# Optimization experiments

Hardware: AMD Instinct MI355X
Metric: run time of the kernel (lower is better)

Reference implementation:

```python
import jax, jax.numpy as jnp
import numpy as np

N, H, C = 16384, 32, 128
RADIUS = 1.0
SIGMA = 1.0
SHELL_SIZES = [1, 14, 28]
EPS = 1e-5


def make_kernel_points(radius, shell_sizes, dim=3, seed=42):
    """Deterministic kernel point dispositions: one center point, then shells of
    unit-direction points at increasing radii (fixed buffer, like load_kernels)."""
    rng = np.random.RandomState(seed)
    shell_radii = np.linspace(0.0, radius, len(shell_sizes))
    pts = [np.zeros((shell_sizes[0], dim))]
    for s, r in zip(shell_sizes[1:], shell_radii[1:]):
        d = rng.randn(s, dim)
        d /= np.linalg.norm(d, axis=1, keepdims=True)
        pts.append(d * r)
    return np.concatenate(pts, 0).astype(np.float32)  # (K, dim)


_KP = jnp.asarray(make_kernel_points(RADIUS, SHELL_SIZES))  # (43, 3)


def batch_norm(x, gamma, beta):
    # BatchNorm1d in training mode over the point/batch axis, biased variance.
    mean = jnp.mean(x, axis=0)
    var = jnp.mean(jnp.square(x - mean), axis=0)
    return (x - mean) * jax.lax.rsqrt(var + EPS) * gamma + beta


def setup_inputs() -> dict:
    key = jax.random.key(0)
    ks = jax.random.split(key, 8)
    coord = jax.random.normal(ks[0], (N, 3), dtype=jnp.float32)
    feat = jax.random.normal(ks[1], (N, C), dtype=jnp.float32)
    offset = jnp.array([N], dtype=jnp.int64)
    reference_index = jax.random.randint(ks[2], (N, H), 0, N, dtype=jnp.int64)
    fc1_w = jax.random.normal(ks[3], (C, C), dtype=jnp.float32) * 0.02
    fc3_w = jax.random.normal(ks[4], (C, C), dtype=jnp.float32) * 0.02
    conv_w = jax.random.normal(ks[5], (43, C), dtype=jnp.float32) * 0.1
    ones = jnp.ones((C,), dtype=jnp.float32)
    zeros = jnp.zeros((C,), dtype=jnp.float32)
    return {
        "coord": coord, "feat": feat, "offset": offset,
        "reference_index": reference_index,
        "fc1_w": fc1_w, "fc3_w": fc3_w, "conv_w": conv_w,
        "g1": ones, "b1": zeros, "g2": ones, "b2": zeros, "g3": ones, "b3": zeros,
    }


def reference(coord, feat, offset, reference_index, fc1_w, fc3_w, conv_w,
              g1, b1, g2, b2, g3, b3):
    identity = feat
    # fc1 -> BN -> ReLU
    x = jax.nn.relu(batch_norm(feat @ fc1_w.T, g1, b1))

    # ---- KPConvD (depthwise kernel point conv, Cmid=0) ----
    # shadow point far away / shadow feature = 0 for out-of-range neighbor index N
    s_pts = jnp.concatenate([coord, jnp.full((1, 3), 1e6, coord.dtype)], axis=0)
    s_feats = jnp.concatenate([x, jnp.zeros((1, C), x.dtype)], axis=0)
    neighbors = s_pts[reference_index] - coord[:, None, :]          # (N, H, 3)
    diff = neighbors[:, :, None, :] - _KP[None, None, :, :]          # (N, H, K, 3)
    sq_d = jnp.sum(diff * diff, axis=-1)                             # (N, H, K)
    infl = jnp.clip(1.0 - jnp.sqrt(sq_d) / SIGMA, 0.0, None)         # (N, H, K) linear influence
    nfeats = s_feats[reference_index]                                # (N, H, C) neighbor gather
    weighted = jnp.einsum('nhk,nhc->nkc', infl, nfeats)              # (N, K, C)
    x = jnp.sum(weighted * conv_w[None], axis=1)                     # depthwise sum over K -> (N, C)

    # BN -> ReLU
    x = jax.nn.relu(batch_norm(x, g2, b2))
    # fc3 -> BN
    x = batch_norm(x @ fc3_w.T, g3, b3)
    # residual + ReLU (drop_path_rate=0 -> identity)
    feat_out = jax.nn.relu(identity + x)
    return coord, feat_out, offset
```

## Files before the change

kernel.cpp:

```cpp
#include <hip/hip_runtime.h>
#include <math.h>

#define NPTS 16384
#define NH   32
#define NC   128
#define NK   43

typedef __attribute__((ext_vector_type(8))) short short8;
typedef __attribute__((ext_vector_type(4))) float f32x4;

enum : int {
  OFF_W1PK = 0,
  OFF_W3PK = 8192,
  OFF_CWPK = 16384,
  OFF_KPF  = 20480,
  OFF_SC1  = 20736, OFF_SH1 = 20864,
  OFF_SC2  = 20992, OFF_SH2 = 21120,
  OFF_SC3  = 21248, OFF_SH3 = 21376,
  OFF_RED  = 21504,
  OFF_CNT  = 29696,
  OFF_PART = 29952,
  OFF_A    = 1078528,
  OFF_B    = 1078528 + NPTS*NC,
};

struct KPArgs { float p[NK * 3]; };

static void host_make_kp(float* kp) {
  unsigned int mt[624];
  mt[0] = 42u;
  for (int i = 1; i < 624; ++i)
    mt[i] = 1812433253u * (mt[i-1] ^ (mt[i-1] >> 30)) + (unsigned)i;
  int pos = 624;
  auto next = [&]() -> unsigned int {
    if (pos == 624) {
      for (int i = 0; i < 624; ++i) {
        unsigned int y = (mt[i] & 0x80000000u) | (mt[(i+1)%624] & 0x7fffffffu);
        unsigned int v = mt[(i+397)%624] ^ (y >> 1);
        if (y & 1u) v ^= 0x9908b0dfu;
        mt[i] = v;
      }
      pos = 0;
    }
    unsigned int y = mt[pos++];
    y ^= y >> 11;
    y ^= (y << 7)  & 0x9d2c5680u;
    y ^= (y << 15) & 0xefc60000u;
    y ^= y >> 18;
    return y;
  };
  auto rdouble = [&]() -> double {
    unsigned int a = next() >> 5, b = next() >> 6;
    return ((double)a * 67108864.0 + (double)b) / 9007199254740992.0;
  };
  double gcache = 0.0; bool has_g = false;
  auto gauss = [&]() -> double {
    if (has_g) { has_g = false; return gcache; }
    double x1, x2, r2;
    do {
      x1 = 2.0 * rdouble() - 1.0;
      x2 = 2.0 * rdouble() - 1.0;
      r2 = x1*x1 + x2*x2;
    } while (r2 >= 1.0 || r2 == 0.0);
    double f = sqrt(-2.0 * log(r2) / r2);
    gcache = f * x1; has_g = true;
    return f * x2;
  };
  double g[126];
  for (int i = 0; i < 126; ++i) g[i] = gauss();
  kp[0] = 0.f; kp[1] = 0.f; kp[2] = 0.f;
  for (int r = 0; r < 14; ++r) {
    double x = g[r*3], y = g[r*3+1], z = g[r*3+2];
    double nrm = sqrt(x*x + y*y + z*z);
    kp[(1+r)*3+0] = (float)(x / nrm * 0.5);
    kp[(1+r)*3+1] = (float)(y / nrm * 0.5);
    kp[(1+r)*3+2] = (float)(z / nrm * 0.5);
  }
  for (int r = 0; r < 28; ++r) {
    double x = g[42+r*3], y = g[42+r*3+1], z = g[42+r*3+2];
    double nrm = sqrt(x*x + y*y + z*z);
    kp[(15+r)*3+0] = (float)(x / nrm);
    kp[(15+r)*3+1] = (float)(y / nrm);
    kp[(15+r)*3+2] = (float)(z / nrm);
  }
}

__device__ __forceinline__ unsigned short f2bf(float f) {
  unsigned u = __float_as_uint(f);
  return (unsigned short)((u + 0x7FFFu + ((u >> 16) & 1u)) >> 16);
}
__device__ __forceinline__ unsigned pack_bf_trunc(float a, float b) {
  return __builtin_amdgcn_perm(__float_as_uint(b), __float_as_uint(a), 0x07060302);
}

__global__ __launch_bounds__(256) void prep_kernel(
    const float* __restrict__ w1, const float* __restrict__ w3,
    const float* __restrict__ cw, KPArgs kpa,
    uint4* __restrict__ w1pk, uint4* __restrict__ w3pk,
    uint4* __restrict__ cwpk, float* __restrict__ kpf,
    unsigned* __restrict__ cnt) {
  int idx = blockIdx.x * 256 + threadIdx.x;
  if (idx == 0) *cnt = 0u;
  if (idx < 4096) {
    int mat = idx >> 11, t = idx & 2047;
    int f = t >> 6, l = t & 63;
    int nt = f >> 2, ks = f & 3;
    int c = nt*16 + (l & 15), k0 = ks*32 + (l >> 4)*8;
    const float* src = mat ? w3 : w1;
    const float* p = src + (size_t)c * NC + k0;
    uint4 q;
    q.x = (unsigned)f2bf(p[0]) | ((unsigned)f2bf(p[1]) << 16);
    q.y = (unsigned)f2bf(p[2]) | ((unsigned)f2bf(p[3]) << 16);
    q.z = (unsigned)f2bf(p[4]) | ((unsigned)f2bf(p[5]) << 16);
    q.w = (unsigned)f2bf(p[6]) | ((unsigned)f2bf(p[7]) << 16);
    (mat ? w3pk : w1pk)[f*64 + l] = q;
  } else if (idx < 4096 + 1024) {
    int t = idx - 4096;
    int f = t >> 6, l = t & 63;
    int ks = f >> 3, nt = f & 7;
    int c = nt*16 + (l & 15), k0 = ks*32 + (l >> 4)*8;
    float v[8];
    #pragma unroll
    for (int i = 0; i < 8; ++i) {
      int k = k0 + i;
      v[i] = (k < NK) ? cw[k*NC + c] : 0.f;
    }
    uint4 q;
    q.x = (unsigned)f2bf(v[0]) | ((unsigned)f2bf(v[1]) << 16);
    q.y = (unsigned)f2bf(v[2]) | ((unsigned)f2bf(v[3]) << 16);
    q.z = (unsigned)f2bf(v[4]) | ((unsigned)f2bf(v[5]) << 16);
    q.w = (unsigned)f2bf(v[6]) | ((unsigned)f2bf(v[7]) << 16);
    cwpk[f*64 + l] = q;
  } else if (idx < 4096 + 1024 + 256) {
    int t = idx - (4096 + 1024);
    int comp = t >> 6, slot = t & 63;
    int ks = slot >> 5, g = (slot >> 3) & 3, i = slot & 7;
    int k = ks*32 + g*8 + i;
    float val;
    if (k < NK) {
      float x = kpa.p[k*3+0], y = kpa.p[k*3+1], z = kpa.p[k*3+2];
      val = (comp == 0) ? -2.f*x : (comp == 1) ? -2.f*y : (comp == 2) ? -2.f*z
            : (x*x + y*y + z*z);
    } else {
      val = (comp == 3) ? 1e12f : 0.f;
    }
    kpf[comp*64 + slot] = val;
  }
}

template<int BN>
__global__ __launch_bounds__(64) void gemm_mfma(
    const float* __restrict__ A, const uint4* __restrict__ Wpk,
    const float* __restrict__ sc, const float* __restrict__ sh,
    float* __restrict__ out, float* __restrict__ part) {
  int l = threadIdx.x;
  int li = l & 15, g = l >> 4;
  const float* arow = A + (size_t)(blockIdx.x * 16 + li) * NC;

  short8 afr[4];
  #pragma unroll
  for (int ks = 0; ks < 4; ++ks) {
    int k0 = ks*32 + g*8;
    float4 a0 = *(const float4*)(arow + k0);
    float4 a1 = *(const float4*)(arow + k0 + 4);
    float v[8] = {a0.x,a0.y,a0.z,a0.w,a1.x,a1.y,a1.z,a1.w};
    if (BN) {
      float4 s0 = *(const float4*)(sc + k0), s1 = *(const float4*)(sc + k0 + 4);
      float4 h0 = *(const float4*)(sh + k0), h1 = *(const float4*)(sh + k0 + 4);
      float ss[8] = {s0.x,s0.y,s0.z,s0.w,s1.x,s1.y,s1.z,s1.w};
      float hh[8] = {h0.x,h0.y,h0.z,h0.w,h1.x,h1.y,h1.z,h1.w};
      #pragma unroll
      for (int i = 0; i < 8; ++i) v[i] = fmaxf(0.f, fmaf(v[i], ss[i], hh[i]));
    }
    union { unsigned q[4]; short8 s; } pk;
    #pragma unroll
    for (int p = 0; p < 4; ++p) pk.q[p] = pack_bf_trunc(v[2*p], v[2*p+1]);
    afr[ks] = pk.s;
  }

  f32x4 acc[8];
  #pragma unroll
  for (int nt = 0; nt < 8; ++nt) acc[nt] = (f32x4){0.f,0.f,0.f,0.f};
  #pragma unroll
  for (int nt = 0; nt < 8; ++nt) {
    #pragma unroll
    for (int ks = 0; ks < 4; ++ks) {
      union { uint4 u; short8 s; } b;
      b.u = Wpk[(nt*4 + ks)*64 + l];
      acc[nt] = __builtin_amdgcn_mfma_f32_16x16x32_bf16(afr[ks], b.s, acc[nt], 0, 0, 0);
    }
  }

  float s[8], q[8];
  #pragma unroll
  for (int nt = 0; nt < 8; ++nt) {
    #pragma unroll
    for (int r = 0; r < 4; ++r)
      out[(size_t)(blockIdx.x*16 + g*4 + r) * NC + nt*16 + li] = acc[nt][r];
    float sv = acc[nt][0]+acc[nt][1]+acc[nt][2]+acc[nt][3];
    float qv = acc[nt][0]*acc[nt][0]+acc[nt][1]*acc[nt][1]
             + acc[nt][2]*acc[nt][2]+acc[nt][3]*acc[nt][3];
    sv += __shfl_xor(sv, 16); sv += __shfl_xor(sv, 32);
    qv += __shfl_xor(qv, 16); qv += __shfl_xor(qv, 32);
    s[nt] = sv; q[nt] = qv;
  }
  if (g == 0) {
    #pragma unroll
    for (int nt = 0; nt < 8; ++nt) {
      part[(size_t)blockIdx.x*256 + nt*16 + li]       = s[nt];
      part[(size_t)blockIdx.x*256 + 128 + nt*16 + li] = q[nt];
    }
  }
}

template<int NB, int NBLK>
__global__ __launch_bounds__(256) void bn_final_mb(
    const float* __restrict__ part,
    const float* __restrict__ g, const float* __restrict__ b,
    float* __restrict__ sc, float* __restrict__ sh,
    float* __restrict__ red, unsigned* __restrict__ cnt) {
  int t = threadIdx.x;
  int blk = blockIdx.x;
  constexpr int PER = NB / NBLK;
  size_t base = (size_t)blk * PER * 256 + t;
  float a0 = 0.f, a1 = 0.f, a2 = 0.f, a3 = 0.f;
  for (int i = 0; i < PER; i += 4) {
    a0 += part[base + (size_t)(i+0)*256];
    a1 += part[base + (size_t)(i+1)*256];
    a2 += part[base + (size_t)(i+2)*256];
    a3 += part[base + (size_t)(i+3)*256];
  }
  red[blk*256 + t] = (a0 + a1) + (a2 + a3);
  __threadfence();
  __shared__ unsigned lastv;
  if (t == 0) lastv = atomicAdd(cnt, 1u);
  __syncthreads();
  if (lastv == (unsigned)(NBLK - 1)) {
    __threadfence();
    float S = 0.f;
    #pragma unroll
    for (int k = 0; k < NBLK; ++k) S += red[k*256 + t];
    __shared__ float fs[256];
    fs[t] = S;
    __syncthreads();
    if (t < 128) {
      double mean = (double)fs[t] * (1.0 / (double)NPTS);
      double var  = (double)fs[128+t] * (1.0 / (double)NPTS) - mean * mean;
      double rstd = 1.0 / sqrt(var + 1e-5);
      double scale = (double)g[t] * rstd;
      sc[t] = (float)scale;
      sh[t] = (float)((double)b[t] - mean * scale);
    }
    if (t == 0) *cnt = 0u;
  }
}

__global__ __launch_bounds__(256) void bn1_pack(
    const float* __restrict__ A, const float* __restrict__ sc,
    const float* __restrict__ sh, unsigned* __restrict__ F) {
  int t = blockIdx.x * 256 + threadIdx.x;
  int n = t >> 4, w = t & 15;
  int c0 = w * 4;
  const float* row = A + (size_t)n * NC;
  float4 a  = *(const float4*)(row + c0);
  float4 bb = *(const float4*)(row + c0 + 64);
  float4 s0 = *(const float4*)(sc + c0), s1 = *(const float4*)(sc + c0 + 64);
  float4 h0 = *(const float4*)(sh + c0), h1 = *(const float4*)(sh + c0 + 64);
  float av[4] = {a.x,a.y,a.z,a.w},   bv[4] = {bb.x,bb.y,bb.z,bb.w};
  float sv0[4] = {s0.x,s0.y,s0.z,s0.w}, sv1[4] = {s1.x,s1.y,s1.z,s1.w};
  float hv0[4] = {h0.x,h0.y,h0.z,h0.w}, hv1[4] = {h1.x,h1.y,h1.z,h1.w};
  unsigned* Fr = F + (size_t)n * 64;
  #pragma unroll
  for (int e = 0; e < 4; ++e) {
    int c = c0 + e, li = c & 15, nt = c >> 4;
    float x = fmaxf(0.f, fmaf(av[e], sv0[e], hv0[e]));
    float y = fmaxf(0.f, fmaf(bv[e], sv1[e], hv1[e]));
    Fr[li*4 + nt] = (unsigned)f2bf(x) | ((unsigned)f2bf(y) << 16);
  }
}

__global__ __launch_bounds__(256) void kpconv_kernel(
    const float* __restrict__ coord, const int* __restrict__ ref,
    const unsigned* __restrict__ F, const uint4* __restrict__ cwpk,
    const float* __restrict__ kpf, float* __restrict__ y,
    float* __restrict__ part)
{
  int l = threadIdx.x & 63, w = threadIdx.x >> 6;
  int g = l >> 4, li = l & 15;
  const uint4* F4 = (const uint4*)F;

  int n = blockIdx.x * 4 + w;
  const int* refrow = ref + (size_t)n * NH;

  int jr0 = refrow[li];
  int jr1 = refrow[16 + li];
  int jh0[4], jh1[4];
  #pragma unroll
  for (int r = 0; r < 4; ++r) { jh0[r] = refrow[g*4 + r]; jh1[r] = refrow[16 + g*4 + r]; }

  union { uint4 u; short8 s; } b0, b1, nb0, nb1;
  b0.u = cwpk[0*64 + l];
  b1.u = cwpk[8*64 + l];

  float cx = coord[n*3+0], cy = coord[n*3+1], cz = coord[n*3+2];
  bool s0r = ((unsigned)jr0 >= (unsigned)NPTS); int j0 = s0r ? 0 : jr0;
  bool s1r = ((unsigned)jr1 >= (unsigned)NPTS); int j1 = s1r ? 0 : jr1;
  float p0x = (s0r ? 1e6f : coord[j0*3+0]) - cx;
  float p0y = (s0r ? 1e6f : coord[j0*3+1]) - cy;
  float p0z = (s0r ? 1e6f : coord[j0*3+2]) - cz;
  float p1x = (s1r ? 1e6f : coord[j1*3+0]) - cx;
  float p1y = (s1r ? 1e6f : coord[j1*3+1]) - cy;
  float p1z = (s1r ? 1e6f : coord[j1*3+2]) - cz;

  uint4 fqA[4], fqB[4];
  #pragma unroll
  for (int r = 0; r < 4; ++r) {
    int jhc = ((unsigned)jh0[r] >= (unsigned)NPTS) ? 0 : jh0[r];
    fqA[r] = F4[(size_t)jhc * 16 + li];
  }
  #pragma unroll
  for (int r = 0; r < 4; ++r) {
    int jhc = ((unsigned)jh1[r] >= (unsigned)NPTS) ? 0 : jh1[r];
    fqB[r] = F4[(size_t)jhc * 16 + li];
  }

  float pp0 = fmaf(p0z, p0z, fmaf(p0y, p0y, p0x*p0x));
  float pp1 = fmaf(p1z, p1z, fmaf(p1y, p1y, p1x*p1x));

  short8 afr[2][2];
  #pragma unroll
  for (int ks = 0; ks < 2; ++ks) {
    const float* kb = kpf + ks*32 + g*8;
    float4 X0 = *(const float4*)(kb +   0), X1 = *(const float4*)(kb +   4);
    float4 Y0 = *(const float4*)(kb +  64), Y1 = *(const float4*)(kb +  68);
    float4 Z0 = *(const float4*)(kb + 128), Z1 = *(const float4*)(kb + 132);
    float4 K0 = *(const float4*)(kb + 192), K1 = *(const float4*)(kb + 196);
    float X[8] = {X0.x,X0.y,X0.z,X0.w,X1.x,X1.y,X1.z,X1.w};
    float Y[8] = {Y0.x,Y0.y,Y0.z,Y0.w,Y1.x,Y1.y,Y1.z,Y1.w};
    float Z[8] = {Z0.x,Z0.y,Z0.z,Z0.w,Z1.x,Z1.y,Z1.z,Z1.w};
    float K[8] = {K0.x,K0.y,K0.z,K0.w,K1.x,K1.y,K1.z,K1.w};
    #pragma unroll
    for (int mt = 0; mt < 2; ++mt) {
      float fx = mt ? p1x : p0x, fy = mt ? p1y : p0y, fz = mt ? p1z : p0z;
      float fp = mt ? pp1 : pp0;
      unsigned u[8];
      #pragma unroll
      for (int i = 0; i < 8; ++i) {
        float d2 = fmaf(fz, Z[i], fmaf(fy, Y[i], fmaf(fx, X[i], fp + K[i])));
        d2 = fmaxf(d2, 0.f);
        float iv = fmaxf(1.f - __builtin_amdgcn_sqrtf(d2), 0.f);
        u[i] = __float_as_uint(iv);
      }
      union { unsigned q[4]; short8 s; } pk;
      #pragma unroll
      for (int p = 0; p < 4; ++p)
        pk.q[p] = __builtin_amdgcn_perm(u[2*p+1], u[2*p], 0x07060302);
      afr[mt][ks] = pk.s;
    }
  }

  f32x4 acc[2][8];
  #pragma unroll
  for (int mt = 0; mt < 2; ++mt)
    #pragma unroll
    for (int nt = 0; nt < 8; ++nt)
      acc[mt][nt] = (f32x4){0.f, 0.f, 0.f, 0.f};

  #pragma unroll
  for (int nt = 0; nt < 8; ++nt) {
    if (nt < 7) {
      nb0.u = cwpk[(nt + 1)*64 + l];
      nb1.u = cwpk[(8 + nt + 1)*64 + l];
    }
    #pragma unroll
    for (int mt = 0; mt < 2; ++mt) {
      acc[mt][nt] = __builtin_amdgcn_mfma_f32_16x16x32_bf16(afr[mt][0], b0.s, acc[mt][nt], 0, 0, 0);
      acc[mt][nt] = __builtin_amdgcn_mfma_f32_16x16x32_bf16(afr[mt][1], b1.s, acc[mt][nt], 0, 0, 0);
    }
    b0 = nb0; b1 = nb1;
  }

  float outp[8];
  #pragma unroll
  for (int p = 0; p < 8; ++p) outp[p] = 0.f;
  #pragma unroll
  for (int mt = 0; mt < 2; ++mt) {
    #pragma unroll
    for (int r = 0; r < 4; ++r) {
      uint4 q = mt ? fqB[r] : fqA[r];
      unsigned uu[4] = {q.x, q.y, q.z, q.w};
      #pragma unroll
      for (int p = 0; p < 4; ++p) {
        float flo = __uint_as_float(uu[p] << 16);
        float fhi = __uint_as_float(uu[p] & 0xffff0000u);
        outp[p]     = fmaf(acc[mt][p][r],     flo, outp[p]);
        outp[p + 4] = fmaf(acc[mt][p + 4][r], fhi, outp[p + 4]);
      }
    }
  }
  #pragma unroll
  for (int p = 0; p < 8; ++p) {
    outp[p] += __shfl_xor(outp[p], 16);
    outp[p] += __shfl_xor(outp[p], 32);
  }
  float o0 = (g == 0) ? outp[0] : (g == 1) ? outp[1] : (g == 2) ? outp[2] : outp[3];
  float o1 = (g == 0) ? outp[4] : (g == 1) ? outp[5] : (g == 2) ? outp[6] : outp[7];
  y[(size_t)n * NC + l]      = o0;
  y[(size_t)n * NC + 64 + l] = o1;

  __shared__ float sl[4][128], ql[4][128];
  sl[w][l] = o0; sl[w][64 + l] = o1;
  ql[w][l] = o0 * o0; ql[w][64 + l] = o1 * o1;
  __syncthreads();
  int t = threadIdx.x;
  int c = t & 127;
  const float (*src)[128] = (t < 128) ? sl : ql;
  part[(size_t)blockIdx.x*256 + t] = (src[0][c] + src[1][c]) + (src[2][c] + src[3][c]);
}

__global__ __launch_bounds__(256) void final_out_kernel(
    const float* __restrict__ feat, const float* __restrict__ z,
    const float* __restrict__ sc, const float* __restrict__ sh,
    const float* __restrict__ coord, const int* __restrict__ offs,
    float* __restrict__ out) {
  int i = blockIdx.x * 256 + threadIdx.x;
  if (i < NPTS * NC / 4) {
    float4 f = ((const float4*)feat)[i];
    float4 v = ((const float4*)z)[i];
    int c = (i & 31) << 2;
    v.x = fmaxf(0.f, f.x + fmaf(v.x, sc[c+0], sh[c+0]));
    v.y = fmaxf(0.f, f.y + fmaf(v.y, sc[c+1], sh[c+1]));
    v.z = fmaxf(0.f, f.z + fmaf(v.z, sc[c+2], sh[c+2]));
    v.w = fmaxf(0.f, f.w + fmaf(v.w, sc[c+3], sh[c+3]));
    ((float4*)out)[NPTS*3/4 + i] = v;
  } else {
    int ci = i - NPTS * NC / 4;
    if (ci < NPTS*3/4) ((float4*)out)[ci] = ((const float4*)coord)[ci];
    if (ci == 0) out[NPTS*3 + (size_t)NPTS*NC] = (float)offs[0];
  }
}

extern "C" void kernel_launch(void* const* d_in, const int* in_sizes, int n_in,
                              void* d_out, int out_size, void* d_ws, size_t ws_size,
                              hipStream_t stream) {
  (void)in_sizes; (void)n_in; (void)out_size; (void)ws_size;
  const float* coord = (const float*)d_in[0];
  const float* feat  = (const float*)d_in[1];
  const int*   offs  = (const int*)d_in[2];
  const int*   ref   = (const int*)d_in[3];
  const float* w1    = (const float*)d_in[4];
  const float* w3    = (const float*)d_in[5];
  const float* cw    = (const float*)d_in[6];
  const float* g1 = (const float*)d_in[7],  *b1 = (const float*)d_in[8];
  const float* g2 = (const float*)d_in[9],  *b2 = (const float*)d_in[10];
  const float* g3 = (const float*)d_in[11], *b3 = (const float*)d_in[12];

  float* ws  = (float*)d_ws;
  float* out = (float*)d_out;
  uint4* w1pk = (uint4*)(ws + OFF_W1PK);
  uint4* w3pk = (uint4*)(ws + OFF_W3PK);
  uint4* cwpk = (uint4*)(ws + OFF_CWPK);
  float* kpf  = ws + OFF_KPF;
  float* sc1 = ws + OFF_SC1, *sh1 = ws + OFF_SH1;
  float* sc2 = ws + OFF_SC2, *sh2 = ws + OFF_SH2;
  float* sc3 = ws + OFF_SC3, *sh3 = ws + OFF_SH3;
  float* red  = ws + OFF_RED;
  unsigned* cnt = (unsigned*)(ws + OFF_CNT);
  float* part = ws + OFF_PART;
  float* A = ws + OFF_A;
  float* B = ws + OFF_B;
  unsigned* F = (unsigned*)(out + NPTS*3);

  KPArgs kpa;
  host_make_kp(kpa.p);

  prep_kernel<<<21, 256, 0, stream>>>(w1, w3, cw, kpa, w1pk, w3pk, cwpk, kpf, cnt);

  gemm_mfma<0><<<NPTS/16, 64, 0, stream>>>(feat, w1pk, nullptr, nullptr, A, part);
  bn_final_mb<1024, 16><<<16, 256, 0, stream>>>(part, g1, b1, sc1, sh1, red, cnt);
  bn1_pack<<<NPTS*16/256, 256, 0, stream>>>(A, sc1, sh1, F);

  kpconv_kernel<<<NPTS/4, 256, 0, stream>>>(coord, ref, F, cwpk, kpf, B, part);
  bn_final_mb<4096, 32><<<32, 256, 0, stream>>>(part, g2, b2, sc2, sh2, red, cnt);

  gemm_mfma<1><<<NPTS/16, 64, 0, stream>>>(B, w3pk, sc2, sh2, A, part);
  bn_final_mb<1024, 16><<<16, 256, 0, stream>>>(part, g3, b3, sc3, sh3, red, cnt);

  final_out_kernel<<<(NPTS*NC/4 + NPTS*3/4 + 255)/256, 256, 0, stream>>>(
      feat, A, sc3, sh3, coord, offs, out);
}
```

Before: 86.99 us.

## Fuse BN1 pack into fc1 GEMM epilogue and apply BN1 in kpconv gather

The fc1 GEMM now writes its raw output directly as packed bf16 in the layout kpconv gathers, which removes the bn1_pack kernel and the fp32 round trip through A. The BN1 scale/shift and ReLU are applied on the fly to gathered neighbour features inside kpconv. The kpconv kernel is split so each wave handles 16 neighbours of one point, with 512-thread blocks and a shared-memory reduction that combines the two halves. The fc3 GEMM splits its output columns across two blocks to raise parallelism. The trade-offs are an extra BN FMA per gathered element and bf16 rounding of pre-BN values rather than post-BN values.

```diff
diff --git a/kernel.cpp b/kernel.cpp
--- a/kernel.cpp
+++ b/kernel.cpp
@@ -148,14 +148,17 @@
   }
 }
 
-template<int BN>
+template<int BN, int PACK, int NSP>
 __global__ __launch_bounds__(64) void gemm_mfma(
     const float* __restrict__ A, const uint4* __restrict__ Wpk,
     const float* __restrict__ sc, const float* __restrict__ sh,
-    float* __restrict__ out, float* __restrict__ part) {
+    float* __restrict__ out, unsigned* __restrict__ Fpk,
+    float* __restrict__ part) {
   int l = threadIdx.x;
   int li = l & 15, g = l >> 4;
-  const float* arow = A + (size_t)(blockIdx.x * 16 + li) * NC;
+  int rt   = (NSP == 1) ? blockIdx.x : (blockIdx.x >> 1);
+  int half = (NSP == 1) ? 0 : (blockIdx.x & 1);
+  const float* arow = A + (size_t)(rt * 16 + li) * NC;
 
   short8 afr[4];
   #pragma unroll
@@ -178,25 +181,42 @@
     afr[ks] = pk.s;
   }
 
-  f32x4 acc[8];
-  #pragma unroll
-  for (int nt = 0; nt < 8; ++nt) acc[nt] = (f32x4){0.f,0.f,0.f,0.f};
-  #pragma unroll
-  for (int nt = 0; nt < 8; ++nt) {
+  constexpr int NT = 8 / NSP;
+  f32x4 acc[NT];
+  #pragma unroll
+  for (int nt = 0; nt < NT; ++nt) acc[nt] = (f32x4){0.f,0.f,0.f,0.f};
+  #pragma unroll
+  for (int nt = 0; nt < NT; ++nt) {
+    int gnt = half*NT + nt;
     #pragma unroll
     for (int ks = 0; ks < 4; ++ks) {
       union { uint4 u; short8 s; } b;
-      b.u = Wpk[(nt*4 + ks)*64 + l];
+      b.u = Wpk[(gnt*4 + ks)*64 + l];
       acc[nt] = __builtin_amdgcn_mfma_f32_16x16x32_bf16(afr[ks], b.s, acc[nt], 0, 0, 0);
     }
   }
 
-  float s[8], q[8];
-  #pragma unroll
-  for (int nt = 0; nt < 8; ++nt) {
-    #pragma unroll
-    for (int r = 0; r < 4; ++r)
-      out[(size_t)(blockIdx.x*16 + g*4 + r) * NC + nt*16 + li] = acc[nt][r];
+  if (PACK) {
+    #pragma unroll
+    for (int r = 0; r < 4; ++r) {
+      uint4 q;
+      q.x = pack_bf_trunc(acc[0][r], acc[4][r]);
+      q.y = pack_bf_trunc(acc[1][r], acc[5][r]);
+      q.z = pack_bf_trunc(acc[2][r], acc[6][r]);
+      q.w = pack_bf_trunc(acc[3][r], acc[7][r]);
+      ((uint4*)(Fpk + (size_t)(rt*16 + g*4 + r) * 64))[li] = q;
+    }
+  } else {
+    #pragma unroll
+    for (int nt = 0; nt < NT; ++nt)
+      #pragma unroll
+      for (int r = 0; r < 4; ++r)
+        out[(size_t)(rt*16 + g*4 + r) * NC + (half*NT + nt)*16 + li] = acc[nt][r];
+  }
+
+  float s[NT], q[NT];
+  #pragma unroll
+  for (int nt = 0; nt < NT; ++nt) {
     float sv = acc[nt][0]+acc[nt][1]+acc[nt][2]+acc[nt][3];
     float qv = acc[nt][0]*acc[nt][0]+acc[nt][1]*acc[nt][1]
              + acc[nt][2]*acc[nt][2]+acc[nt][3]*acc[nt][3];
@@ -206,9 +226,10 @@
   }
   if (g == 0) {
     #pragma unroll
-    for (int nt = 0; nt < 8; ++nt) {
-      part[(size_t)blockIdx.x*256 + nt*16 + li]       = s[nt];
-      part[(size_t)blockIdx.x*256 + 128 + nt*16 + li] = q[nt];
+    for (int nt = 0; nt < NT; ++nt) {
+      int c = (half*NT + nt)*16 + li;
+      part[(size_t)rt*256 + c]       = s[nt];
+      part[(size_t)rt*256 + 128 + c] = q[nt];
     }
   }
 }
@@ -255,79 +276,53 @@
   }
 }
 
-__global__ __launch_bounds__(256) void bn1_pack(
-    const float* __restrict__ A, const float* __restrict__ sc,
-    const float* __restrict__ sh, unsigned* __restrict__ F) {
-  int t = blockIdx.x * 256 + threadIdx.x;
-  int n = t >> 4, w = t & 15;
-  int c0 = w * 4;
-  const float* row = A + (size_t)n * NC;
-  float4 a  = *(const float4*)(row + c0);
-  float4 bb = *(const float4*)(row + c0 + 64);
-  float4 s0 = *(const float4*)(sc + c0), s1 = *(const float4*)(sc + c0 + 64);
-  float4 h0 = *(const float4*)(sh + c0), h1 = *(const float4*)(sh + c0 + 64);
-  float av[4] = {a.x,a.y,a.z,a.w},   bv[4] = {bb.x,bb.y,bb.z,bb.w};
-  float sv0[4] = {s0.x,s0.y,s0.z,s0.w}, sv1[4] = {s1.x,s1.y,s1.z,s1.w};
-  float hv0[4] = {h0.x,h0.y,h0.z,h0.w}, hv1[4] = {h1.x,h1.y,h1.z,h1.w};
-  unsigned* Fr = F + (size_t)n * 64;
-  #pragma unroll
-  for (int e = 0; e < 4; ++e) {
-    int c = c0 + e, li = c & 15, nt = c >> 4;
-    float x = fmaxf(0.f, fmaf(av[e], sv0[e], hv0[e]));
-    float y = fmaxf(0.f, fmaf(bv[e], sv1[e], hv1[e]));
-    Fr[li*4 + nt] = (unsigned)f2bf(x) | ((unsigned)f2bf(y) << 16);
-  }
-}
-
-__global__ __launch_bounds__(256) void kpconv_kernel(
+__global__ __launch_bounds__(512) void kpconv_kernel(
     const float* __restrict__ coord, const int* __restrict__ ref,
     const unsigned* __restrict__ F, const uint4* __restrict__ cwpk,
-    const float* __restrict__ kpf, float* __restrict__ y,
-    float* __restrict__ part)
+    const float* __restrict__ kpf,
+    const float* __restrict__ sc1, const float* __restrict__ sh1,
+    float* __restrict__ y, float* __restrict__ part)
 {
-  int l = threadIdx.x & 63, w = threadIdx.x >> 6;
+  __shared__ float sl[8][128];
+  __shared__ float cl[4][128];
+  int tid = threadIdx.x;
+  int l = tid & 63, w = tid >> 6;
   int g = l >> 4, li = l & 15;
+  int pt = w >> 1, mt = w & 1;
   const uint4* F4 = (const uint4*)F;
 
-  int n = blockIdx.x * 4 + w;
-  const int* refrow = ref + (size_t)n * NH;
-
-  int jr0 = refrow[li];
-  int jr1 = refrow[16 + li];
-  int jh0[4], jh1[4];
-  #pragma unroll
-  for (int r = 0; r < 4; ++r) { jh0[r] = refrow[g*4 + r]; jh1[r] = refrow[16 + g*4 + r]; }
+  int n = blockIdx.x * 4 + pt;
+  const int* refrow = ref + (size_t)n * NH + mt*16;
+
+  int jr = refrow[li];
+  int jh[4];
+  #pragma unroll
+  for (int r = 0; r < 4; ++r) jh[r] = refrow[g*4 + r];
 
   union { uint4 u; short8 s; } b0, b1, nb0, nb1;
   b0.u = cwpk[0*64 + l];
   b1.u = cwpk[8*64 + l];
 
   float cx = coord[n*3+0], cy = coord[n*3+1], cz = coord[n*3+2];
-  bool s0r = ((unsigned)jr0 >= (unsigned)NPTS); int j0 = s0r ? 0 : jr0;
-  bool s1r = ((unsigned)jr1 >= (unsigned)NPTS); int j1 = s1r ? 0 : jr1;
-  float p0x = (s0r ? 1e6f : coord[j0*3+0]) - cx;
-  float p0y = (s0r ? 1e6f : coord[j0*3+1]) - cy;
-  float p0z = (s0r ? 1e6f : coord[j0*3+2]) - cz;
-  float p1x = (s1r ? 1e6f : coord[j1*3+0]) - cx;
-  float p1y = (s1r ? 1e6f : coord[j1*3+1]) - cy;
-  float p1z = (s1r ? 1e6f : coord[j1*3+2]) - cz;
-
-  uint4 fqA[4], fqB[4];
+  bool shad = ((unsigned)jr >= (unsigned)NPTS); int j0 = shad ? 0 : jr;
+  float px = (shad ? 1e6f : coord[j0*3+0]) - cx;
+  float py = (shad ? 1e6f : coord[j0*3+1]) - cy;
+  float pz = (shad ? 1e6f : coord[j0*3+2]) - cz;
+
+  uint4 fq[4];
   #pragma unroll
   for (int r = 0; r < 4; ++r) {
-    int jhc = ((unsigned)jh0[r] >= (unsigned)NPTS) ? 0 : jh0[r];
-    fqA[r] = F4[(size_t)jhc * 16 + li];
-  }
-  #pragma unroll
-  for (int r = 0; r < 4; ++r) {
-    int jhc = ((unsigned)jh1[r] >= (unsigned)NPTS) ? 0 : jh1[r];
-    fqB[r] = F4[(size_t)jhc * 16 + li];
-  }
-
-  float pp0 = fmaf(p0z, p0z, fmaf(p0y, p0y, p0x*p0x));
-  float pp1 = fmaf(p1z, p1z, fmaf(p1y, p1y, p1x*p1x));
-
-  short8 afr[2][2];
+    int jhc = ((unsigned)jh[r] >= (unsigned)NPTS) ? 0 : jh[r];
+    fq[r] = F4[(size_t)jhc * 16 + li];
+  }
+
+  float s1[8], h1[8];
+  #pragma unroll
+  for (int p = 0; p < 8; ++p) { s1[p] = sc1[p*16 + li]; h1[p] = sh1[p*16 + li]; }
+
+  float pp = fmaf(pz, pz, fmaf(py, py, px*px));
+
+  short8 afr[2];
   #pragma unroll
   for (int ks = 0; ks < 2; ++ks) {
     const float* kb = kpf + ks*32 + g*8;
@@ -339,44 +334,32 @@
     float Y[8] = {Y0.x,Y0.y,Y0.z,Y0.w,Y1.x,Y1.y,Y1.z,Y1.w};
     float Z[8] = {Z0.x,Z0.y,Z0.z,Z0.w,Z1.x,Z1.y,Z1.z,Z1.w};
     float K[8] = {K0.x,K0.y,K0.z,K0.w,K1.x,K1.y,K1.z,K1.w};
-    #pragma unroll
-    for (int mt = 0; mt < 2; ++mt) {
-      float fx = mt ? p1x : p0x, fy = mt ? p1y : p0y, fz = mt ? p1z : p0z;
-      float fp = mt ? pp1 : pp0;
-      unsigned u[8];
-      #pragma unroll
-      for (int i = 0; i < 8; ++i) {
-        float d2 = fmaf(fz, Z[i], fmaf(fy, Y[i], fmaf(fx, X[i], fp + K[i])));
-        d2 = fmaxf(d2, 0.f);
-        float iv = fmaxf(1.f - __builtin_amdgcn_sqrtf(d2), 0.f);
-        u[i] = __float_as_uint(iv);
-      }
-      union { unsigned q[4]; short8 s; } pk;
-      #pragma unroll
-      for (int p = 0; p < 4; ++p)
-        pk.q[p] = __builtin_amdgcn_perm(u[2*p+1], u[2*p], 0x07060302);
-      afr[mt][ks] = pk.s;
-    }
-  }
-
-  f32x4 acc[2][8];
-  #pragma unroll
-  for (int mt = 0; mt < 2; ++mt)
-    #pragma unroll
-    for (int nt = 0; nt < 8; ++nt)
-      acc[mt][nt] = (f32x4){0.f, 0.f, 0.f, 0.f};
-
+    unsigned u[8];
+    #pragma unroll
+    for (int i = 0; i < 8; ++i) {
+      float d2 = fmaf(pz, Z[i], fmaf(py, Y[i], fmaf(px, X[i], pp + K[i])));
+      d2 = fmaxf(d2, 0.f);
+      float iv = fmaxf(1.f - __builtin_amdgcn_sqrtf(d2), 0.f);
+      u[i] = __float_as_uint(iv);
+    }
+    union { unsigned q[4]; short8 s; } pk;
+    #pragma unroll
+    for (int p = 0; p < 4; ++p)
+      pk.q[p] = __builtin_amdgcn_perm(u[2*p+1], u[2*p], 0x07060302);
+    afr[ks] = pk.s;
+  }
+
+  f32x4 acc[8];
+  #pragma unroll
+  for (int nt = 0; nt < 8; ++nt) acc[nt] = (f32x4){0.f, 0.f, 0.f, 0.f};
   #pragma unroll
   for (int nt = 0; nt < 8; ++nt) {
     if (nt < 7) {
       nb0.u = cwpk[(nt + 1)*64 + l];
       nb1.u = cwpk[(8 + nt + 1)*64 + l];
     }
-    #pragma unroll
-    for (int mt = 0; mt < 2; ++mt) {
-      acc[mt][nt] = __builtin_amdgcn_mfma_f32_16x16x32_bf16(afr[mt][0], b0.s, acc[mt][nt], 0, 0, 0);
-      acc[mt][nt] = __builtin_amdgcn_mfma_f32_16x16x32_bf16(afr[mt][1], b1.s, acc[mt][nt], 0, 0, 0);
-    }
+    acc[nt] = __builtin_amdgcn_mfma_f32_16x16x32_bf16(afr[0], b0.s, acc[nt], 0, 0, 0);
+    acc[nt] = __builtin_amdgcn_mfma_f32_16x16x32_bf16(afr[1], b1.s, acc[nt], 0, 0, 0);
     b0 = nb0; b1 = nb1;
   }
 
@@ -384,18 +367,16 @@
   #pragma unroll
   for (int p = 0; p < 8; ++p) outp[p] = 0.f;
   #pragma unroll
-  for (int mt = 0; mt < 2; ++mt) {
-    #pragma unroll
-    for (int r = 0; r < 4; ++r) {
-      uint4 q = mt ? fqB[r] : fqA[r];
-      unsigned uu[4] = {q.x, q.y, q.z, q.w};
-      #pragma unroll
-      for (int p = 0; p < 4; ++p) {
-        float flo = __uint_as_float(uu[p] << 16);
-        float fhi = __uint_as_float(uu[p] & 0xffff0000u);
-        outp[p]     = fmaf(acc[mt][p][r],     flo, outp[p]);
-        outp[p + 4] = fmaf(acc[mt][p + 4][r], fhi, outp[p + 4]);
-      }
+  for (int r = 0; r < 4; ++r) {
+    unsigned uu[4] = {fq[r].x, fq[r].y, fq[r].z, fq[r].w};
+    #pragma unroll
+    for (int p = 0; p < 4; ++p) {
+      float flo = __uint_as_float(uu[p] << 16);
+      float fhi = __uint_as_float(uu[p] & 0xffff0000u);
+      flo = fmaxf(0.f, fmaf(flo, s1[p],     h1[p]));
+      fhi = fmaxf(0.f, fmaf(fhi, s1[p + 4], h1[p + 4]));
+      outp[p]     = fmaf(acc[p][r],     flo, outp[p]);
+      outp[p + 4] = fmaf(acc[p + 4][r], fhi, outp[p + 4]);
     }
   }
   #pragma unroll
@@ -405,17 +386,24 @@
   }
   float o0 = (g == 0) ? outp[0] : (g == 1) ? outp[1] : (g == 2) ? outp[2] : outp[3];
   float o1 = (g == 0) ? outp[4] : (g == 1) ? outp[5] : (g == 2) ? outp[6] : outp[7];
-  y[(size_t)n * NC + l]      = o0;
-  y[(size_t)n * NC + 64 + l] = o1;
-
-  __shared__ float sl[4][128], ql[4][128];
-  sl[w][l] = o0; sl[w][64 + l] = o1;
-  ql[w][l] = o0 * o0; ql[w][64 + l] = o1 * o1;
+
+  sl[w][l]      = o0;
+  sl[w][64 + l] = o1;
   __syncthreads();
-  int t = threadIdx.x;
-  int c = t & 127;
-  const float (*src)[128] = (t < 128) ? sl : ql;
-  part[(size_t)blockIdx.x*256 + t] = (src[0][c] + src[1][c]) + (src[2][c] + src[3][c]);
+  {
+    int p2 = tid >> 7, c = tid & 127;
+    float v = sl[2*p2][c] + sl[2*p2+1][c];
+    y[(size_t)(blockIdx.x*4 + p2) * NC + c] = v;
+    cl[p2][c] = v;
+  }
+  __syncthreads();
+  if (tid < 256) {
+    int c = tid & 127;
+    float a0 = cl[0][c], a1 = cl[1][c], a2 = cl[2][c], a3 = cl[3][c];
+    part[(size_t)blockIdx.x*256 + tid] =
+        (tid < 128) ? ((a0 + a1) + (a2 + a3))
+                    : ((a0*a0 + a1*a1) + (a2*a2 + a3*a3));
+  }
 }
 
 __global__ __launch_bounds__(256) void final_out_kernel(
@@ -476,14 +464,15 @@
 
   prep_kernel<<<21, 256, 0, stream>>>(w1, w3, cw, kpa, w1pk, w3pk, cwpk, kpf, cnt);
 
-  gemm_mfma<0><<<NPTS/16, 64, 0, stream>>>(feat, w1pk, nullptr, nullptr, A, part);
+  gemm_mfma<0,1,1><<<NPTS/16, 64, 0, stream>>>(feat, w1pk, nullptr, nullptr,
+                                               nullptr, F, part);
   bn_final_mb<1024, 16><<<16, 256, 0, stream>>>(part, g1, b1, sc1, sh1, red, cnt);
-  bn1_pack<<<NPTS*16/256, 256, 0, stream>>>(A, sc1, sh1, F);
-
-  kpconv_kernel<<<NPTS/4, 256, 0, stream>>>(coord, ref, F, cwpk, kpf, B, part);
+
+  kpconv_kernel<<<NPTS/4, 512, 0, stream>>>(coord, ref, F, cwpk, kpf,
+                                            sc1, sh1, B, part);
   bn_final_mb<4096, 32><<<32, 256, 0, stream>>>(part, g2, b2, sc2, sh2, red, cnt);
 
-  gemm_mfma<1><<<NPTS/16, 64, 0, stream>>>(B, w3pk, sc2, sh2, A, part);
+  gemm_mfma<1,0,2><<<NPTS/8, 64, 0, stream>>>(B, w3pk, sc2, sh2, A, nullptr, part);
   bn_final_mb<1024, 16><<<16, 256, 0, stream>>>(part, g3, b3, sc3, sh3, red, cnt);
 
   final_out_kernel<<<(NPTS*NC/4 + NPTS*3/4 + 255)/256, 256, 0, stream>>>(
```

Measured after the change: 95.90 us. 10.2% more time.

## Fuse bn1 pack into fc1 GEMM epilogue and apply BN1 in kpconv gather

Applied to the files above, without the earlier changes.

The fc1 GEMM now writes raw pre-BN outputs directly as packed bf16 in the gather layout, and the separate bn1_pack pass is removed. The BN1 scale/shift and ReLU are applied inside kpconv after each neighbor feature is unpacked. This drops one kernel launch and a full fp32 write and read of the fc1 output. The fc3 GEMM is also split into two blocks per row tile, each handling half the output columns, to raise parallelism. In exchange, kpconv does extra FMAs on every gathered feature, and BN is applied after bf16 truncation of raw values, which slightly changes rounding.

```diff
diff --git a/kernel.cpp b/kernel.cpp
--- a/kernel.cpp
+++ b/kernel.cpp
@@ -148,14 +148,17 @@
   }
 }
 
-template<int BN>
+template<int BN, int PACK, int NSP>
 __global__ __launch_bounds__(64) void gemm_mfma(
     const float* __restrict__ A, const uint4* __restrict__ Wpk,
     const float* __restrict__ sc, const float* __restrict__ sh,
-    float* __restrict__ out, float* __restrict__ part) {
+    float* __restrict__ out, unsigned* __restrict__ Fpk,
+    float* __restrict__ part) {
   int l = threadIdx.x;
   int li = l & 15, g = l >> 4;
-  const float* arow = A + (size_t)(blockIdx.x * 16 + li) * NC;
+  int rt   = (NSP == 1) ? blockIdx.x : (blockIdx.x >> 1);
+  int half = (NSP == 1) ? 0 : (blockIdx.x & 1);
+  const float* arow = A + (size_t)(rt * 16 + li) * NC;
 
   short8 afr[4];
   #pragma unroll
@@ -178,25 +181,42 @@
     afr[ks] = pk.s;
   }
 
-  f32x4 acc[8];
-  #pragma unroll
-  for (int nt = 0; nt < 8; ++nt) acc[nt] = (f32x4){0.f,0.f,0.f,0.f};
-  #pragma unroll
-  for (int nt = 0; nt < 8; ++nt) {
+  constexpr int NT = 8 / NSP;
+  f32x4 acc[NT];
+  #pragma unroll
+  for (int nt = 0; nt < NT; ++nt) acc[nt] = (f32x4){0.f,0.f,0.f,0.f};
+  #pragma unroll
+  for (int nt = 0; nt < NT; ++nt) {
+    int gnt = half*NT + nt;
     #pragma unroll
     for (int ks = 0; ks < 4; ++ks) {
       union { uint4 u; short8 s; } b;
-      b.u = Wpk[(nt*4 + ks)*64 + l];
+      b.u = Wpk[(gnt*4 + ks)*64 + l];
       acc[nt] = __builtin_amdgcn_mfma_f32_16x16x32_bf16(afr[ks], b.s, acc[nt], 0, 0, 0);
     }
   }
 
-  float s[8], q[8];
-  #pragma unroll
-  for (int nt = 0; nt < 8; ++nt) {
-    #pragma unroll
-    for (int r = 0; r < 4; ++r)
-      out[(size_t)(blockIdx.x*16 + g*4 + r) * NC + nt*16 + li] = acc[nt][r];
+  if (PACK) {
+    #pragma unroll
+    for (int r = 0; r < 4; ++r) {
+      uint4 q;
+      q.x = pack_bf_trunc(acc[0][r], acc[4][r]);
+      q.y = pack_bf_trunc(acc[1][r], acc[5][r]);
+      q.z = pack_bf_trunc(acc[2][r], acc[6][r]);
+      q.w = pack_bf_trunc(acc[3][r], acc[7][r]);
+      ((uint4*)(Fpk + (size_t)(rt*16 + g*4 + r) * 64))[li] = q;
+    }
+  } else {
+    #pragma unroll
+    for (int nt = 0; nt < NT; ++nt)
+      #pragma unroll
+      for (int r = 0; r < 4; ++r)
+        out[(size_t)(rt*16 + g*4 + r) * NC + (half*NT + nt)*16 + li] = acc[nt][r];
+  }
+
+  float s[NT], q[NT];
+  #pragma unroll
+  for (int nt = 0; nt < NT; ++nt) {
     float sv = acc[nt][0]+acc[nt][1]+acc[nt][2]+acc[nt][3];
     float qv = acc[nt][0]*acc[nt][0]+acc[nt][1]*acc[nt][1]
              + acc[nt][2]*acc[nt][2]+acc[nt][3]*acc[nt][3];
@@ -206,9 +226,10 @@
   }
   if (g == 0) {
     #pragma unroll
-    for (int nt = 0; nt < 8; ++nt) {
-      part[(size_t)blockIdx.x*256 + nt*16 + li]       = s[nt];
-      part[(size_t)blockIdx.x*256 + 128 + nt*16 + li] = q[nt];
+    for (int nt = 0; nt < NT; ++nt) {
+      int c = (half*NT + nt)*16 + li;
+      part[(size_t)rt*256 + c]       = s[nt];
+      part[(size_t)rt*256 + 128 + c] = q[nt];
     }
   }
 }
@@ -255,35 +276,12 @@
   }
 }
 
-__global__ __launch_bounds__(256) void bn1_pack(
-    const float* __restrict__ A, const float* __restrict__ sc,
-    const float* __restrict__ sh, unsigned* __restrict__ F) {
-  int t = blockIdx.x * 256 + threadIdx.x;
-  int n = t >> 4, w = t & 15;
-  int c0 = w * 4;
-  const float* row = A + (size_t)n * NC;
-  float4 a  = *(const float4*)(row + c0);
-  float4 bb = *(const float4*)(row + c0 + 64);
-  float4 s0 = *(const float4*)(sc + c0), s1 = *(const float4*)(sc + c0 + 64);
-  float4 h0 = *(const float4*)(sh + c0), h1 = *(const float4*)(sh + c0 + 64);
-  float av[4] = {a.x,a.y,a.z,a.w},   bv[4] = {bb.x,bb.y,bb.z,bb.w};
-  float sv0[4] = {s0.x,s0.y,s0.z,s0.w}, sv1[4] = {s1.x,s1.y,s1.z,s1.w};
-  float hv0[4] = {h0.x,h0.y,h0.z,h0.w}, hv1[4] = {h1.x,h1.y,h1.z,h1.w};
-  unsigned* Fr = F + (size_t)n * 64;
-  #pragma unroll
-  for (int e = 0; e < 4; ++e) {
-    int c = c0 + e, li = c & 15, nt = c >> 4;
-    float x = fmaxf(0.f, fmaf(av[e], sv0[e], hv0[e]));
-    float y = fmaxf(0.f, fmaf(bv[e], sv1[e], hv1[e]));
-    Fr[li*4 + nt] = (unsigned)f2bf(x) | ((unsigned)f2bf(y) << 16);
-  }
-}
-
 __global__ __launch_bounds__(256) void kpconv_kernel(
     const float* __restrict__ coord, const int* __restrict__ ref,
     const unsigned* __restrict__ F, const uint4* __restrict__ cwpk,
-    const float* __restrict__ kpf, float* __restrict__ y,
-    float* __restrict__ part)
+    const float* __restrict__ kpf,
+    const float* __restrict__ sc1, const float* __restrict__ sh1,
+    float* __restrict__ y, float* __restrict__ part)
 {
   int l = threadIdx.x & 63, w = threadIdx.x >> 6;
   int g = l >> 4, li = l & 15;
@@ -323,6 +321,10 @@
     int jhc = ((unsigned)jh1[r] >= (unsigned)NPTS) ? 0 : jh1[r];
     fqB[r] = F4[(size_t)jhc * 16 + li];
   }
+
+  float s1[8], h1[8];
+  #pragma unroll
+  for (int p = 0; p < 8; ++p) { s1[p] = sc1[p*16 + li]; h1[p] = sh1[p*16 + li]; }
 
   float pp0 = fmaf(p0z, p0z, fmaf(p0y, p0y, p0x*p0x));
   float pp1 = fmaf(p1z, p1z, fmaf(p1y, p1y, p1x*p1x));
@@ -393,6 +395,8 @@
       for (int p = 0; p < 4; ++p) {
         float flo = __uint_as_float(uu[p] << 16);
         float fhi = __uint_as_float(uu[p] & 0xffff0000u);
+        flo = fmaxf(0.f, fmaf(flo, s1[p],     h1[p]));
+        fhi = fmaxf(0.f, fmaf(fhi, s1[p + 4], h1[p + 4]));
         outp[p]     = fmaf(acc[mt][p][r],     flo, outp[p]);
         outp[p + 4] = fmaf(acc[mt][p + 4][r], fhi, outp[p + 4]);
       }
@@ -476,14 +480,15 @@
 
   prep_kernel<<<21, 256, 0, stream>>>(w1, w3, cw, kpa, w1pk, w3pk, cwpk, kpf, cnt);
 
-  gemm_mfma<0><<<NPTS/16, 64, 0, stream>>>(feat, w1pk, nullptr, nullptr, A, part);
+  gemm_mfma<0,1,1><<<NPTS/16, 64, 0, stream>>>(feat, w1pk, nullptr, nullptr,
+                                               nullptr, F, part);
   bn_final_mb<1024, 16><<<16, 256, 0, stream>>>(part, g1, b1, sc1, sh1, red, cnt);
-  bn1_pack<<<NPTS*16/256, 256, 0, stream>>>(A, sc1, sh1, F);
-
-  kpconv_kernel<<<NPTS/4, 256, 0, stream>>>(coord, ref, F, cwpk, kpf, B, part);
+
+  kpconv_kernel<<<NPTS/4, 256, 0, stream>>>(coord, ref, F, cwpk, kpf,
+                                            sc1, sh1, B, part);
   bn_final_mb<4096, 32><<<32, 256, 0, stream>>>(part, g2, b2, sc2, sh2, red, cnt);
 
-  gemm_mfma<1><<<NPTS/16, 64, 0, stream>>>(B, w3pk, sc2, sh2, A, part);
+  gemm_mfma<1,0,2><<<NPTS/8, 64, 0, stream>>>(B, w3pk, sc2, sh2, A, nullptr, part);
   bn_final_mb<1024, 16><<<16, 256, 0, stream>>>(part, g3, b3, sc3, sh3, red, cnt);
 
   final_out_kernel<<<(NPTS*NC/4 + NPTS*3/4 + 255)/256, 256, 0, stream>>>(
```

Result: faster. 83.84 us (-3.6%).
